# Optimization experiments

Hardware: AMD Instinct MI355X
Metric: run time of the kernel (lower is better)

Reference implementation:

```python
import jax, jax.numpy as jnp
import numpy as np

T, N, C, S = 512, 32, 8000, 40
BLANK = 0
LOG_TINY = float(np.log(np.finfo(np.float32).tiny))  # matches torch.log(zeros+tiny)


def _expand_with_blank(targets, blank):
    # (N,S) -> (N, 2S+1): [blank, t0, blank, t1, ..., blank]
    n, s = targets.shape
    b = jnp.full((n, s, 1), blank, targets.dtype)
    et = jnp.concatenate([b, targets[:, :, None]], axis=-1).reshape(n, 2 * s)
    et = jnp.concatenate([et, jnp.full((n, 1), blank, targets.dtype)], axis=-1)
    return et


def _log_add(a, b):
    x = jnp.maximum(a, b)
    y = jnp.minimum(a, b)
    return x + jnp.log1p(jnp.exp(y - x))


def setup_inputs() -> dict:
    key = jax.random.key(0)
    k1, k2, k3 = jax.random.split(key, 3)
    log_probs = jax.nn.log_softmax(
        jax.random.normal(k1, (T, N, C), dtype=jnp.float32), axis=-1)
    targets = jax.random.randint(k2, (N, S), 1, C, dtype=jnp.int32)  # non-blank
    input_lengths = jnp.full((N,), T, dtype=jnp.int32)
    target_lengths = jax.random.randint(k3, (N,), 10, S + 1, dtype=jnp.int32)
    return {"log_probs": log_probs, "targets": targets,
            "input_lengths": input_lengths, "target_lengths": target_lengths}


def reference(log_probs, targets, input_lengths, target_lengths):
    # NOTE: original torch code ignores input_lengths (always iterates all T).
    et = _expand_with_blank(targets, BLANK)            # (N, Se), Se = 2S+1
    n, se = et.shape

    alpha0 = jnp.full((n, se), LOG_TINY, dtype=log_probs.dtype)
    alpha0 = alpha0.at[:, 0].set(log_probs[0, :, BLANK])
    alpha0 = alpha0.at[:, 1].set(
        jnp.take_along_axis(log_probs[0], et[:, 1:2], axis=1)[:, 0])

    # skip transition allowed when label differs from label two slots back
    mask_skip = (et[:, 2:] != et[:, :-2]).astype(log_probs.dtype)  # (N, Se-2)
    mask_not = 1.0 - mask_skip

    def step(alpha, lp_t):
        # alpha: (N, Se), lp_t: (N, C)
        np1 = _log_add(alpha[:, 1:], alpha[:, :-1])                 # (N, Se-1)
        np2 = _log_add(np1[:, 1:], alpha[:, :-2]) * mask_skip + np1[:, 1:] * mask_not
        new = jnp.concatenate([alpha[:, :1], np1[:, :1], np2], axis=1)
        alpha = new + jnp.take_along_axis(lp_t, et, axis=1)
        return alpha, None

    alpha, _ = jax.lax.scan(step, alpha0, log_probs[1:])

    lengths = 2 * target_lengths + 1                   # (N,)
    a_last = jnp.take_along_axis(alpha, (lengths - 1)[:, None], axis=1)[:, 0]
    a_prev = jnp.take_along_axis(alpha, (lengths - 2)[:, None], axis=1)[:, 0]
    loss = _log_add(a_last, a_prev)
    # reduction='mean' in this impl: per-sample normalized, no batch mean
    return -(loss / target_lengths.astype(log_probs.dtype))
```

## Files before the change

kernel.cpp:

```cpp
#include <hip/hip_runtime.h>
#include <math.h>

#define T_STEPS 512
#define N_BATCH 32
#define C_CLS   8000
#define S_TGT   40

#define LOG_TINY (-87.3365447505531f)

__device__ __forceinline__ float log_add(float a, float b) {
    float x = fmaxf(a, b);
    float y = fminf(a, b);
    return x + __logf(1.0f + __expf(y - x));
}

extern "C" __global__ __launch_bounds__(64)
void ctc_fwd(const float* __restrict__ lp,
             const int*   __restrict__ targets,
             const int*   __restrict__ in_len,
             const int*   __restrict__ tgt_len,
             float*       __restrict__ out) {
    const int n = blockIdx.x;
    const int l = threadIdx.x;

    int cls = 0;
    if (l < S_TGT) cls = targets[n * S_TGT + l];
    int prev_cls = __shfl_up(cls, 1);
    const bool skip = (l >= 1 && l < S_TGT) && (cls != prev_cls);

    const float* row0 = lp + (size_t)n * C_CLS;
    float a_e, a_o;
    if (l == 0) { a_e = row0[0]; a_o = row0[cls]; }
    else        { a_e = LOG_TINY; a_o = LOG_TINY; }

    const size_t rstride = (size_t)N_BATCH * C_CLS;
    constexpr int P = 7;
    float pb[P], pt[P];
#pragma unroll
    for (int i = 0; i < P; ++i) {
        const float* row = lp + (size_t)(1 + i) * rstride + (size_t)n * C_CLS;
        pb[i] = row[0];
        pt[i] = row[cls];
    }

    int t = 1;
    for (int outer = 0; outer < (T_STEPS - 1) / P; ++outer) {
#pragma unroll
        for (int i = 0; i < P; ++i) {
            float lpb = pb[i], lpt = pt[i];
            int tn = t + P; if (tn > T_STEPS - 1) tn = T_STEPS - 1;
            const float* rown = lp + (size_t)tn * rstride + (size_t)n * C_CLS;
            pb[i] = rown[0];
            pt[i] = rown[cls];

            float up_o = __shfl_up(a_o, 1);
            float ne = (l == 0) ? a_e : log_add(a_e, up_o);
            float bo = log_add(a_o, a_e);
            bo = skip ? log_add(bo, up_o) : bo;
            a_e = ne + lpb;
            a_o = bo + lpt;
            ++t;
        }
    }

    const int TL = tgt_len[n];
    float v1 = __shfl(a_e, TL);
    float v2 = __shfl(a_o, TL - 1);
    if (l == 0) {
        float loss = log_add(v1, v2);
        out[n] = -loss / (float)TL;
    }
    (void)in_len;
}

extern "C" void kernel_launch(void* const* d_in, const int* in_sizes, int n_in,
                              void* d_out, int out_size, void* d_ws, size_t ws_size,
                              hipStream_t stream) {
    const float* lp  = (const float*)d_in[0];
    const int*   tg  = (const int*)d_in[1];
    const int*   il  = (const int*)d_in[2];
    const int*   tl  = (const int*)d_in[3];
    float*       out = (float*)d_out;
    hipLaunchKernelGGL(ctc_fwd, dim3(N_BATCH), dim3(64), 0, stream,
                       lp, tg, il, tl, out);
}
```

Before: 774.9 us.

## Pre-gather target log-probs into packed workspace before serial CTC recurrence

Adds a massively parallel gather kernel that pulls each (t, n) blank and target log-prob out of the large log_probs tensor into a compact per-sample workspace of 48 floats per timestep. The serial recurrence kernel then streams this contiguous packed array, so each step's global load is one coalesced load instead of scattered gathers. The blank value is read through a lane shuffle. The pairwise log-add chain is also rewritten as a fused three-way log-sum-exp to shorten the dependency chain. The cost is an extra kernel launch and a workspace round trip.

```diff
diff --git a/kernel.cpp b/kernel.cpp
--- a/kernel.cpp
+++ b/kernel.cpp
@@ -5,72 +5,84 @@
 #define N_BATCH 32
 #define C_CLS   8000
 #define S_TGT   40
+#define ROW     48
+#define LOG_TINY (-87.3365447505531f)
+#define NEG_BIG  (-1.0e30f)
 
-#define LOG_TINY (-87.3365447505531f)
-
-__device__ __forceinline__ float log_add(float a, float b) {
-    float x = fmaxf(a, b);
-    float y = fminf(a, b);
-    return x + __logf(1.0f + __expf(y - x));
+extern "C" __global__ __launch_bounds__(64)
+void ctc_gather(const float* __restrict__ lp,
+                const int*   __restrict__ targets,
+                float*       __restrict__ packed) {
+    const int t = blockIdx.x;
+    const int n = blockIdx.y;
+    const int l = threadIdx.x;
+    if (l > 40) return;
+    const int cls = (l < S_TGT) ? targets[n * S_TGT + l] : 0;
+    const float v = lp[((size_t)t * N_BATCH + n) * C_CLS + cls];
+    packed[((size_t)n * T_STEPS + t) * ROW + l] = v;
 }
 
 extern "C" __global__ __launch_bounds__(64)
-void ctc_fwd(const float* __restrict__ lp,
+void ctc_rec(const float* __restrict__ packed,
              const int*   __restrict__ targets,
-             const int*   __restrict__ in_len,
              const int*   __restrict__ tgt_len,
              float*       __restrict__ out) {
     const int n = blockIdx.x;
     const int l = threadIdx.x;
 
-    int cls = 0;
-    if (l < S_TGT) cls = targets[n * S_TGT + l];
-    int prev_cls = __shfl_up(cls, 1);
-    const bool skip = (l >= 1 && l < S_TGT) && (cls != prev_cls);
+    const int cls      = (l < S_TGT) ? targets[n * S_TGT + l] : 0;
+    const int prev_cls = __shfl_up(cls, 1);
+    const bool skip    = (l >= 1 && l < S_TGT) && (cls != prev_cls);
 
-    const float* row0 = lp + (size_t)n * C_CLS;
+    const float* base = packed + (size_t)n * T_STEPS * ROW;
+    const int ll = (l <= 40) ? l : 40;
+
     float a_e, a_o;
-    if (l == 0) { a_e = row0[0]; a_o = row0[cls]; }
-    else        { a_e = LOG_TINY; a_o = LOG_TINY; }
+    {
+        const float v0 = base[ll];
+        const float b0 = __shfl(v0, 40);
+        a_e = (l == 0) ? b0 : LOG_TINY;
+        a_o = (l == 0) ? v0 : LOG_TINY;
+    }
 
-    const size_t rstride = (size_t)N_BATCH * C_CLS;
     constexpr int P = 7;
-    float pb[P], pt[P];
+    float pv[P];
 #pragma unroll
-    for (int i = 0; i < P; ++i) {
-        const float* row = lp + (size_t)(1 + i) * rstride + (size_t)n * C_CLS;
-        pb[i] = row[0];
-        pt[i] = row[cls];
-    }
+    for (int i = 0; i < P; ++i) pv[i] = base[(1 + i) * ROW + ll];
 
     int t = 1;
     for (int outer = 0; outer < (T_STEPS - 1) / P; ++outer) {
 #pragma unroll
         for (int i = 0; i < P; ++i) {
-            float lpb = pb[i], lpt = pt[i];
+            const float v = pv[i];
             int tn = t + P; if (tn > T_STEPS - 1) tn = T_STEPS - 1;
-            const float* rown = lp + (size_t)tn * rstride + (size_t)n * C_CLS;
-            pb[i] = rown[0];
-            pt[i] = rown[cls];
+            pv[i] = base[tn * ROW + ll];
 
-            float up_o = __shfl_up(a_o, 1);
-            float ne = (l == 0) ? a_e : log_add(a_e, up_o);
-            float bo = log_add(a_o, a_e);
-            bo = skip ? log_add(bo, up_o) : bo;
-            a_e = ne + lpb;
-            a_o = bo + lpt;
+            const float lpb  = __shfl(v, 40);
+            const float up_o = __shfl_up(a_o, 1);
+
+            const float ue = (l == 0) ? NEG_BIG : up_o;
+            const float m2 = fmaxf(a_e, ue);
+            const float ne = m2 + __logf(__expf(a_e - m2) + __expf(ue - m2)) + lpb;
+
+            const float c  = skip ? up_o : NEG_BIG;
+            const float m3 = fmaxf(fmaxf(a_o, a_e), c);
+            const float no = m3 + __logf(__expf(a_o - m3) + __expf(a_e - m3)
+                                         + __expf(c - m3)) + v;
+            a_e = ne;
+            a_o = no;
             ++t;
         }
     }
 
     const int TL = tgt_len[n];
-    float v1 = __shfl(a_e, TL);
-    float v2 = __shfl(a_o, TL - 1);
+    const float v1 = __shfl(a_e, TL);
+    const float v2 = __shfl(a_o, TL - 1);
     if (l == 0) {
-        float loss = log_add(v1, v2);
+        const float x = fmaxf(v1, v2), y = fminf(v1, v2);
+        const float loss = x + __logf(1.0f + __expf(y - x));
         out[n] = -loss / (float)TL;
     }
-    (void)in_len;
 }
 
 extern "C" void kernel_launch(void* const* d_in, const int* in_sizes, int n_in,
@@ -78,9 +90,12 @@
                               hipStream_t stream) {
     const float* lp  = (const float*)d_in[0];
     const int*   tg  = (const int*)d_in[1];
-    const int*   il  = (const int*)d_in[2];
     const int*   tl  = (const int*)d_in[3];
     float*       out = (float*)d_out;
-    hipLaunchKernelGGL(ctc_fwd, dim3(N_BATCH), dim3(64), 0, stream,
-                       lp, tg, il, tl, out);
+    float*       packed = (float*)d_ws;
+
+    hipLaunchKernelGGL(ctc_gather, dim3(T_STEPS, N_BATCH), dim3(64), 0, stream,
+                       lp, tg, packed);
+    hipLaunchKernelGGL(ctc_rec, dim3(N_BATCH), dim3(64), 0, stream,
+                       packed, tg, tl, out);
 }
```

Result: faster. 651.5 us (-15.9%).
